# Kernel optimization log

Measured on AMD Instinct MI355X. Metric: run time of the kernel, lower is better.

## Reference

```python
import jax, jax.numpy as jnp
import numpy as np

C = 256
G = 32  # groups
EPS = 1e-5

def _xavier(key, shape, gain=1.0):
    fan_in, fan_out = shape[1], shape[0]
    a = gain * np.sqrt(6.0 / (fan_in + fan_out))
    return jax.random.uniform(key, shape, jnp.float32, -a, a)

def setup_inputs() -> dict:
    key = jax.random.key(0)
    ks = jax.random.split(key, 5)
    x = jax.random.normal(ks[0], (2, C, 16, 16, 16), jnp.float32)
    return {
        "x": x,
        "gn_gamma": jnp.ones((C,), jnp.float32),
        "gn_beta": jnp.zeros((C,), jnp.float32),
        "Wq": _xavier(ks[1], (C, C)), "bq": jnp.zeros((C,), jnp.float32),
        "Wk": _xavier(ks[2], (C, C)), "bk": jnp.zeros((C,), jnp.float32),
        "Wv": _xavier(ks[3], (C, C)), "bv": jnp.zeros((C,), jnp.float32),
        "Wp": _xavier(ks[4], (C, C), gain=1e-05), "bp": jnp.zeros((C,), jnp.float32),
    }

def reference(x, gn_gamma, gn_beta, Wq, bq, Wk, bk, Wv, bv, Wp, bp):
    B, Cc, D, H, W = x.shape
    N = D * H * W
    xf = x.reshape(B, Cc, N)  # [B, C, N]
    # GroupNorm over (C//G, N) per group
    xg = xf.reshape(B, G, Cc // G, N)
    mu = jnp.mean(xg, axis=(2, 3), keepdims=True)
    var = jnp.var(xg, axis=(2, 3), keepdims=True)
    h = ((xg - mu) * jax.lax.rsqrt(var + EPS)).reshape(B, Cc, N)
    h = h * gn_gamma[None, :, None] + gn_beta[None, :, None]
    # 1x1x1 convs == channel matmuls
    q = jnp.einsum('oc,bcn->bno', Wq, h) + bq  # [B, N, C]
    k = jnp.einsum('oc,bcn->bon', Wk, h) + bk[None, :, None]  # [B, C, N]
    v = jnp.einsum('oc,bcn->bno', Wv, h) + bv  # [B, N, C]
    scale = float(Cc) ** (-0.5)
    w = jnp.einsum('bnc,bcm->bnm', q, k) * scale  # [B, N, N]
    w = jax.nn.softmax(w, axis=-1)
    a = jnp.einsum('bnm,bmc->bnc', w, v)  # [B, N, C]
    out = jnp.einsum('oc,bnc->bon', Wp, a) + bp[None, :, None]  # [B, C, N]
    return x + out.reshape(B, Cc, D, H, W)
```

## Files before the change

### kernel.cpp

```cpp
#include <hip/hip_runtime.h>
#include <stdint.h>

#define B_ 2
#define C_ 256
#define N_ 4096
#define EPS_ 1e-5f

typedef short short8 __attribute__((ext_vector_type(8)));
typedef float f32x4 __attribute__((ext_vector_type(4)));
typedef float f32x16 __attribute__((ext_vector_type(16)));
typedef long long i64;

static __device__ __forceinline__ unsigned short f2bf(float f) {
    union { float f; unsigned int u; } v; v.f = f;
    unsigned int r = v.u + 0x7FFF + ((v.u >> 16) & 1);
    return (unsigned short)(r >> 16);
}
static __device__ __forceinline__ float bf2f(unsigned short u) {
    union { unsigned int u; float f; } v; v.u = ((unsigned int)u) << 16;
    return v.f;
}
static __device__ __forceinline__ unsigned char f2fp8(float f) {
    return (unsigned char)(__builtin_amdgcn_cvt_pk_fp8_f32(f, f, 0, false) & 0xff);
}
static __device__ __forceinline__ unsigned int pack4_bf8(float a, float b, float c, float d) {
    int v = __builtin_amdgcn_cvt_pk_bf8_f32(a, b, 0, false);
    v = __builtin_amdgcn_cvt_pk_bf8_f32(c, d, v, true);
    return (unsigned int)v;
}
static __device__ __forceinline__ i64 mk64(unsigned int lo, unsigned int hi) {
    return (i64)(((unsigned long long)hi << 32) | (unsigned long long)lo);
}

__global__ __launch_bounds__(256) void prep(
    const float* __restrict__ x, float2* __restrict__ stats,
    const float* __restrict__ Wq, const float* __restrict__ Wk,
    const float* __restrict__ Wv, const float* __restrict__ Wp,
    ushort* __restrict__ o)
{
    __shared__ float as_[4], as2_[4];
    if (blockIdx.x < 64) {
        const float4* p = reinterpret_cast<const float4*>(x + (size_t)blockIdx.x * 32768);
        float s = 0.f, ss = 0.f;
        for (int i = threadIdx.x; i < 8192; i += 256) {
            float4 v = p[i];
            s  += v.x + v.y + v.z + v.w;
            ss += v.x*v.x + v.y*v.y + v.z*v.z + v.w*v.w;
        }
        for (int m = 32; m; m >>= 1) { s += __shfl_down(s, m, 64); ss += __shfl_down(ss, m, 64); }
        int w = threadIdx.x >> 6;
        if ((threadIdx.x & 63) == 0) { as_[w] = s; as2_[w] = ss; }
        __syncthreads();
        if (threadIdx.x == 0) {
            float S = as_[0]+as_[1]+as_[2]+as_[3], SS = as2_[0]+as2_[1]+as2_[2]+as2_[3];
            float mu = S / 32768.f;
            float var = SS / 32768.f - mu*mu;
            stats[blockIdx.x] = make_float2(mu, rsqrtf(var + EPS_));
        }
    } else {
        int t = (blockIdx.x - 64) * 256 + threadIdx.x;
        int idx = t * 4;
        int sel = idx >> 16;
        const float* src = sel == 0 ? Wq : sel == 1 ? Wk : sel == 2 ? Wv : Wp;
        float4 v = *reinterpret_cast<const float4*>(src + (idx & 65535));
        ushort4 r; r.x = f2bf(v.x); r.y = f2bf(v.y); r.z = f2bf(v.z); r.w = f2bf(v.w);
        *reinterpret_cast<ushort4*>(o + idx) = r;
    }
}

__global__ void gnorm_t(const float* __restrict__ x, const float2* __restrict__ stats,
                        const float* __restrict__ gamma, const float* __restrict__ beta,
                        ushort* __restrict__ ht) {
    __shared__ float tile[32][33];
    int b = blockIdx.z, n0 = blockIdx.x * 32, c0 = blockIdx.y * 32;
    int tx = threadIdx.x, ty = threadIdx.y;
    #pragma unroll
    for (int i = 0; i < 4; i++) {
        int c = c0 + ty + i*8;
        float2 st = stats[b*32 + (c >> 3)];
        float v = x[((size_t)(b*C_ + c))*N_ + n0 + tx];
        tile[ty + i*8][tx] = (v - st.x) * st.y * gamma[c] + beta[c];
    }
    __syncthreads();
    #pragma unroll
    for (int i = 0; i < 4; i++) {
        int n = n0 + ty + i*8;
        ht[((size_t)(b*N_ + n))*C_ + c0 + tx] = f2bf(tile[tx][ty + i*8]);
    }
}

__global__ __launch_bounds__(256) void qkvproj(
    const ushort* __restrict__ ht, const ushort* __restrict__ wq,
    const ushort* __restrict__ wk, const ushort* __restrict__ wv,
    const float* __restrict__ bq, const float* __restrict__ bk, const float* __restrict__ bv,
    unsigned char* __restrict__ qo, unsigned char* __restrict__ ko, unsigned char* __restrict__ vo)
{
    __shared__ ushort sA[64][72], sBq[64][72], sBk[64][72], sBv[64][72];
    int bz = blockIdx.z;
    const ushort* Ab = ht + (size_t)bz * N_ * C_;
    int i0 = blockIdx.x * 64, j0 = blockIdx.y * 64;
    int tid = threadIdx.x, w = tid >> 6, lane = tid & 63, lr = lane & 15, lg = lane >> 4;
    f32x4 aq[4] = {}, ak[4] = {}, av[4] = {};
    for (int ks = 0; ks < 256; ks += 64) {
        #pragma unroll
        for (int it = 0; it < 2; it++) {
            int ch = tid + it*256;
            int row = ch >> 3, cc = ch & 7;
            *reinterpret_cast<uint4*>(&sA[row][cc*8]) =
                *reinterpret_cast<const uint4*>(Ab + ((size_t)(i0 + row))*256 + ks + cc*8);
            *reinterpret_cast<uint4*>(&sBq[row][cc*8]) =
                *reinterpret_cast<const uint4*>(wq + ((size_t)(j0 + row))*256 + ks + cc*8);
            *reinterpret_cast<uint4*>(&sBk[row][cc*8]) =
                *reinterpret_cast<const uint4*>(wk + ((size_t)(j0 + row))*256 + ks + cc*8);
            *reinterpret_cast<uint4*>(&sBv[row][cc*8]) =
                *reinterpret_cast<const uint4*>(wv + ((size_t)(j0 + row))*256 + ks + cc*8);
        }
        __syncthreads();
        #pragma unroll
        for (int kc = 0; kc < 2; kc++) {
            short8 af = *reinterpret_cast<const short8*>(&sA[w*16 + lr][kc*32 + lg*8]);
            #pragma unroll
            for (int cb = 0; cb < 4; cb++) {
                short8 b1 = *reinterpret_cast<const short8*>(&sBq[cb*16 + lr][kc*32 + lg*8]);
                short8 b2 = *reinterpret_cast<const short8*>(&sBk[cb*16 + lr][kc*32 + lg*8]);
                short8 b3 = *reinterpret_cast<const short8*>(&sBv[cb*16 + lr][kc*32 + lg*8]);
                aq[cb] = __builtin_amdgcn_mfma_f32_16x16x32_bf16(af, b1, aq[cb], 0, 0, 0);
                ak[cb] = __builtin_amdgcn_mfma_f32_16x16x32_bf16(af, b2, ak[cb], 0, 0, 0);
                av[cb] = __builtin_amdgcn_mfma_f32_16x16x32_bf16(af, b3, av[cb], 0, 0, 0);
            }
        }
        __syncthreads();
    }
    #pragma unroll
    for (int cb = 0; cb < 4; cb++) {
        #pragma unroll
        for (int r = 0; r < 4; r++) {
            int i = i0 + w*16 + lg*4 + r;
            int j = j0 + cb*16 + lr;
            size_t oidx = ((size_t)(bz*N_ + i))*256 + j;
            qo[oidx] = f2fp8(aq[cb][r] + bq[j]);
            ko[oidx] = f2fp8(ak[cb][r] + bk[j]);
            vo[((size_t)bz*C_ + j)*N_ + i] = f2fp8(av[cb][r] + bv[j]);
        }
    }
}

#define FLASH_LDS 70656
__global__ __launch_bounds__(256, 2) void flash10(
    const unsigned char* __restrict__ q, const unsigned char* __restrict__ k,
    const unsigned char* __restrict__ vT,
    ushort* __restrict__ Opart, float* __restrict__ lsum, ushort* __restrict__ aout, int nsplit)
{
    extern __shared__ char smem[];
    int b = blockIdx.z, s = blockIdx.y, qt = blockIdx.x;
    int tid = threadIdx.x, w = tid >> 6, lane = tid & 63;
    int l31 = lane & 31, hi = lane >> 5;
    int nrow0 = qt*128 + w*32;
    const unsigned char* kB = k  + (size_t)b * N_ * 256;
    const unsigned char* vB = vT + (size_t)b * 256 * N_;

    i64 qf[16];
    #pragma unroll
    for (int kc = 0; kc < 16; kc++)
        qf[kc] = *reinterpret_cast<const i64*>(
            q + ((size_t)(b*N_) + nrow0 + l31)*256 + kc*16 + hi*8);

    f32x16 oacc[8] = {};
    float lp = 0.f;

    int tiles = 64 / nsplit;
    int t0 = s * tiles;

    char* kbuf0 = smem;
    char* vbuf0 = smem + 33792;

    int koff[4], kd[4], voff[4], vd[4];
    #pragma unroll
    for (int i = 0; i < 4; i++) {
        int row = w*16 + i*4 + (lane >> 4);
        koff[i] = (t0*64 + row)*256 + (lane & 15)*16;
        kd[i]   = row*264 + (lane & 15)*16;
        int c = w*64 + i*16 + (lane >> 2);
        voff[i] = c*4096 + t0*64 + (lane & 3)*16;
        vd[i]   = c*72 + (lane & 3)*16;
    }

    uint4 kreg[4], vreg[4];
    auto loadKV = [&]() {
        #pragma unroll
        for (int i = 0; i < 4; i++) { kreg[i] = *reinterpret_cast<const uint4*>(kB + koff[i]); koff[i] += 16384; }
        #pragma unroll
        for (int i = 0; i < 4; i++) { vreg[i] = *reinterpret_cast<const uint4*>(vB + voff[i]); voff[i] += 64; }
    };
    auto writeKV = [&](int sel) {
        #pragma unroll
        for (int i = 0; i < 4; i++) {
            char* p = kbuf0 + sel*16896 + kd[i];
            *reinterpret_cast<uint2*>(p)     = make_uint2(kreg[i].x, kreg[i].y);
            *reinterpret_cast<uint2*>(p + 8) = make_uint2(kreg[i].z, kreg[i].w);
        }
        #pragma unroll
        for (int i = 0; i < 4; i++) {
            char* p = vbuf0 + sel*18432 + vd[i];
            *reinterpret_cast<uint2*>(p)     = make_uint2(vreg[i].x, vreg[i].y);
            *reinterpret_cast<uint2*>(p + 8) = make_uint2(vreg[i].z, vreg[i].w);
        }
    };

    loadKV();
    writeKV(0);
    __syncthreads();
    int sel = 0;

    for (int ti = 0; ti < tiles; ti++) {
        bool more = (ti + 1 < tiles);
        if (more) loadKV();

        const char* kb_ = kbuf0 + sel*16896;
        f32x16 s0 = {}, s1 = {};
        __builtin_amdgcn_s_setprio(1);
        #pragma unroll
        for (int kc = 0; kc < 16; kc++) {
            i64 ka0 = *reinterpret_cast<const i64*>(kb_ + l31*264        + kc*16 + hi*8);
            i64 ka1 = *reinterpret_cast<const i64*>(kb_ + (l31+32)*264   + kc*16 + hi*8);
            s0 = __builtin_amdgcn_mfma_f32_32x32x16_fp8_fp8(ka0, qf[kc], s0, 0, 0, 0);
            s1 = __builtin_amdgcn_mfma_f32_32x32x16_fp8_fp8(ka1, qf[kc], s1, 0, 0, 0);
        }
        __builtin_amdgcn_s_setprio(0);

        float e0[16], e1[16];
        #pragma unroll
        for (int r = 0; r < 16; r++) {
            e0[r] = __expf(fminf(s0[r]*0.0625f, 10.5f));
            e1[r] = __expf(fminf(s1[r]*0.0625f, 10.5f));
            lp += e0[r] + e1[r];
        }
        unsigned p0 = pack4_bf8(e0[0],e0[1],e0[2],e0[3]);
        unsigned p1 = pack4_bf8(e0[4],e0[5],e0[6],e0[7]);
        unsigned p2 = pack4_bf8(e0[8],e0[9],e0[10],e0[11]);
        unsigned p3 = pack4_bf8(e0[12],e0[13],e0[14],e0[15]);
        unsigned t0_ = pack4_bf8(e1[0],e1[1],e1[2],e1[3]);
        unsigned t1_ = pack4_bf8(e1[4],e1[5],e1[6],e1[7]);
        unsigned t2_ = pack4_bf8(e1[8],e1[9],e1[10],e1[11]);
        unsigned t3_ = pack4_bf8(e1[12],e1[13],e1[14],e1[15]);
        unsigned xp0 = (unsigned)__shfl_xor((int)p0, 32, 64);
        unsigned xp1 = (unsigned)__shfl_xor((int)p1, 32, 64);
        unsigned xp2 = (unsigned)__shfl_xor((int)p2, 32, 64);
        unsigned xp3 = (unsigned)__shfl_xor((int)p3, 32, 64);
        unsigned xt0 = (unsigned)__shfl_xor((int)t0_, 32, 64);
        unsigned xt1 = (unsigned)__shfl_xor((int)t1_, 32, 64);
        unsigned xt2 = (unsigned)__shfl_xor((int)t2_, 32, 64);
        unsigned xt3 = (unsigned)__shfl_xor((int)t3_, 32, 64);
        i64 A0 = mk64(hi ? xp1 : p0,  hi ? p1 : xp0);
        i64 A1 = mk64(hi ? xp3 : p2,  hi ? p3 : xp2);
        i64 A2 = mk64(hi ? xt1 : t0_, hi ? t1_ : xt0);
        i64 A3 = mk64(hi ? xt3 : t2_, hi ? t3_ : xt2);

        const char* vb_ = vbuf0 + sel*18432;
        __builtin_amdgcn_s_setprio(1);
        #pragma unroll
        for (int cb = 0; cb < 8; cb++) {
            const char* vrow = vb_ + (cb*32 + l31)*72;
            i64 bv0 = *reinterpret_cast<const i64*>(vrow + 0*16  + hi*8);
            oacc[cb] = __builtin_amdgcn_mfma_f32_32x32x16_bf8_fp8(A0, bv0, oacc[cb], 0, 0, 0);
            i64 bv1 = *reinterpret_cast<const i64*>(vrow + 1*16  + hi*8);
            oacc[cb] = __builtin_amdgcn_mfma_f32_32x32x16_bf8_fp8(A1, bv1, oacc[cb], 0, 0, 0);
            i64 bv2 = *reinterpret_cast<const i64*>(vrow + 2*16  + hi*8);
            oacc[cb] = __builtin_amdgcn_mfma_f32_32x32x16_bf8_fp8(A2, bv2, oacc[cb], 0, 0, 0);
            i64 bv3 = *reinterpret_cast<const i64*>(vrow + 3*16  + hi*8);
            oacc[cb] = __builtin_amdgcn_mfma_f32_32x32x16_bf8_fp8(A3, bv3, oacc[cb], 0, 0, 0);
        }
        __builtin_amdgcn_s_setprio(0);

        if (more) writeKV(sel ^ 1);
        __syncthreads();
        sel ^= 1;
    }

    lp += __shfl_xor(lp, 32, 64);

    if (nsplit == 1) {
        float inv = 1.f / lp;
        #pragma unroll
        for (int r = 0; r < 16; r++) {
            int R = (r & 3) + 8*(r >> 2) + 4*hi;
            #pragma unroll
            for (int cb = 0; cb < 8; cb++)
                aout[((size_t)(b*N_) + nrow0 + R)*256 + cb*32 + l31] = f2bf(oacc[cb][r] * inv);
        }
    } else {
        size_t obase = ((size_t)(b*nsplit + s)*N_ + nrow0) * 256;
        #pragma unroll
        for (int r = 0; r < 16; r++) {
            int R = (r & 3) + 8*(r >> 2) + 4*hi;
            #pragma unroll
            for (int cb = 0; cb < 8; cb++)
                Opart[obase + (size_t)R*256 + cb*32 + l31] = f2bf(oacc[cb][r]);
        }
        if (hi == 0)
            lsum[(size_t)(b*nsplit + s)*N_ + nrow0 + l31] = lp;
    }
}

__global__ void combine2(const ushort* __restrict__ Opart, const float* __restrict__ lsum,
                         ushort* __restrict__ aout, int nsplit) {
    int g = threadIdx.x >> 6, lane = threadIdx.x & 63;
    int idx = blockIdx.x*4 + g;
    int b = idx >> 12, n = idx & 4095;
    float L = 0.f;
    for (int s2 = 0; s2 < nsplit; s2++) L += lsum[(size_t)(b*nsplit + s2)*N_ + n];
    float inv = 1.f / L;
    float a0 = 0.f, a1 = 0.f, a2 = 0.f, a3 = 0.f;
    for (int s2 = 0; s2 < nsplit; s2++) {
        ushort4 o = *reinterpret_cast<const ushort4*>(
            Opart + ((size_t)(b*nsplit + s2)*N_ + n)*256 + lane*4);
        a0 += bf2f(o.x); a1 += bf2f(o.y); a2 += bf2f(o.z); a3 += bf2f(o.w);
    }
    ushort4 r; r.x = f2bf(a0*inv); r.y = f2bf(a1*inv); r.z = f2bf(a2*inv); r.w = f2bf(a3*inv);
    *reinterpret_cast<ushort4*>(aout + (size_t)idx*256 + lane*4) = r;
}

__global__ __launch_bounds__(256) void pgemm(
    const ushort* __restrict__ A, const ushort* __restrict__ Bm,
    const float* __restrict__ bias, const float* __restrict__ resid,
    float* __restrict__ outp, long bBatch, long oBatch)
{
    __shared__ ushort sA[64][72];
    __shared__ ushort sB[64][72];
    int bz = blockIdx.z;
    const ushort* Bb = Bm + (size_t)bBatch * bz;
    int i0 = blockIdx.x * 64, j0 = blockIdx.y * 64;
    int tid = threadIdx.x, w = tid >> 6, lane = tid & 63, lr = lane & 15, lg = lane >> 4;
    f32x4 acc[4] = {};
    for (int ks = 0; ks < 256; ks += 64) {
        #pragma unroll
        for (int it = 0; it < 2; it++) {
            int ch = tid + it*256;
            int row = ch >> 3, cc = ch & 7;
            *reinterpret_cast<uint4*>(&sA[row][cc*8]) =
                *reinterpret_cast<const uint4*>(A + ((size_t)(i0 + row))*256 + ks + cc*8);
            *reinterpret_cast<uint4*>(&sB[row][cc*8]) =
                *reinterpret_cast<const uint4*>(Bb + ((size_t)(j0 + row))*256 + ks + cc*8);
        }
        __syncthreads();
        #pragma unroll
        for (int kc = 0; kc < 2; kc++) {
            short8 af = *reinterpret_cast<const short8*>(&sA[w*16 + lr][kc*32 + lg*8]);
            #pragma unroll
            for (int cb = 0; cb < 4; cb++) {
                short8 bf = *reinterpret_cast<const short8*>(&sB[cb*16 + lr][kc*32 + lg*8]);
                acc[cb] = __builtin_amdgcn_mfma_f32_16x16x32_bf16(af, bf, acc[cb], 0, 0, 0);
            }
        }
        __syncthreads();
    }
    #pragma unroll
    for (int cb = 0; cb < 4; cb++) {
        #pragma unroll
        for (int r = 0; r < 4; r++) {
            int i = i0 + w*16 + lg*4 + r;
            int j = j0 + cb*16 + lr;
            size_t oidx = (size_t)oBatch*bz + (size_t)i*N_ + j;
            outp[oidx] = acc[cb][r] + bias[i] + resid[oidx];
        }
    }
}

extern "C" void kernel_launch(void* const* d_in, const int* in_sizes, int n_in,
                              void* d_out, int out_size, void* d_ws, size_t ws_size,
                              hipStream_t stream) {
    const float* x     = (const float*)d_in[0];
    const float* gamma = (const float*)d_in[1];
    const float* beta  = (const float*)d_in[2];
    const float* Wq = (const float*)d_in[3]; const float* bq = (const float*)d_in[4];
    const float* Wk = (const float*)d_in[5]; const float* bk = (const float*)d_in[6];
    const float* Wv = (const float*)d_in[7]; const float* bv = (const float*)d_in[8];
    const float* Wp = (const float*)d_in[9]; const float* bp = (const float*)d_in[10];
    float* out = (float*)d_out;

    char* ws = (char*)d_ws;
    float2* stats = (float2*)ws;
    ushort* wqb = (ushort*)(ws + 1024);
    ushort* wkb = wqb + 65536;
    ushort* wvb = wkb + 65536;
    ushort* wpb = wvb + 65536;
    ushort* ht  = (ushort*)(ws + 1024 + 524288);
    const size_t NB = (size_t)B_ * N_ * C_;
    unsigned char* qb  = (unsigned char*)(ht + NB);
    unsigned char* kb8 = qb  + NB;
    unsigned char* vTb = kb8 + NB;
    ushort* ab = (ushort*)(vTb + NB);
    char* after = (char*)(ab + NB);
    float*  lsum  = (float*)after;
    ushort* Opart = (ushort*)(after + 262144);

    int nsplit = (ws_size >= (size_t)48*1024*1024) ? 8 : 4;

    hipFuncSetAttribute((const void*)flash10, hipFuncAttributeMaxDynamicSharedMemorySize,
                        FLASH_LDS);

    prep<<<320, 256, 0, stream>>>(x, stats, Wq, Wk, Wv, Wp, wqb);
    gnorm_t<<<dim3(128, 8, 2), dim3(32, 8), 0, stream>>>(x, stats, gamma, beta, ht);
    qkvproj<<<dim3(64, 4, 2), 256, 0, stream>>>(ht, wqb, wkb, wvb, bq, bk, bv, qb, kb8, vTb);
    flash10<<<dim3(32, nsplit, 2), 256, FLASH_LDS, stream>>>(qb, kb8, vTb, Opart, lsum, ab, nsplit);
    combine2<<<2048, 256, 0, stream>>>(Opart, lsum, ab, nsplit);
    pgemm<<<dim3(4, 64, 2), 256, 0, stream>>>(wpb, ab, bp, x, out, (long)N_*C_, (long)C_*N_);
}
```

Measured before the change: 87.48 us.

## Interleave QK and PV halves in flash loop, use exp2, stage V transpose in LDS

The flash kernel now computes the two 32-key score halves separately, so exp and PV MMA for the first half can overlap with work on the second. The setprio hints are removed, and the exp is rewritten as exp2f with a folded log2e scale. The nsplit==1 path is dropped. In qkvproj, the transposed V output is staged through an LDS tile so it is written as coalesced 16-byte stores instead of scattered single-byte stores.

Measured after the change: 85.05 us. 2.8% less time.

```diff
diff --git a/kernel.cpp b/kernel.cpp
--- a/kernel.cpp
+++ b/kernel.cpp
@@ -31,6 +31,8 @@
 static __device__ __forceinline__ i64 mk64(unsigned int lo, unsigned int hi) {
     return (i64)(((unsigned long long)hi << 32) | (unsigned long long)lo);
 }
+#define EXPSCALE 0.09016844f
+#define EXPCLAMP 15.148f
 
 __global__ __launch_bounds__(256) void prep(
     const float* __restrict__ x, float2* __restrict__ stats,
@@ -96,6 +98,7 @@
     unsigned char* __restrict__ qo, unsigned char* __restrict__ ko, unsigned char* __restrict__ vo)
 {
     __shared__ ushort sA[64][72], sBq[64][72], sBk[64][72], sBv[64][72];
+    __shared__ __align__(16) unsigned char vtile[64*80];
     int bz = blockIdx.z;
     const ushort* Ab = ht + (size_t)bz * N_ * C_;
     int i0 = blockIdx.x * 64, j0 = blockIdx.y * 64;
@@ -140,16 +143,22 @@
             size_t oidx = ((size_t)(bz*N_ + i))*256 + j;
             qo[oidx] = f2fp8(aq[cb][r] + bq[j]);
             ko[oidx] = f2fp8(ak[cb][r] + bk[j]);
-            vo[((size_t)bz*C_ + j)*N_ + i] = f2fp8(av[cb][r] + bv[j]);
-        }
+            vtile[(cb*16 + lr)*80 + (w*16 + lg*4 + r)] = f2fp8(av[cb][r] + bv[j]);
+        }
+    }
+    __syncthreads();
+    {
+        int cl = tid >> 2, chk = (tid & 3) * 16;
+        uint4 vv = *reinterpret_cast<const uint4*>(&vtile[cl*80 + chk]);
+        *reinterpret_cast<uint4*>(vo + ((size_t)bz*C_ + j0 + cl)*N_ + i0 + chk) = vv;
     }
 }
 
 #define FLASH_LDS 70656
-__global__ __launch_bounds__(256, 2) void flash10(
+__global__ __launch_bounds__(256, 2) void flash11(
     const unsigned char* __restrict__ q, const unsigned char* __restrict__ k,
     const unsigned char* __restrict__ vT,
-    ushort* __restrict__ Opart, float* __restrict__ lsum, ushort* __restrict__ aout, int nsplit)
+    ushort* __restrict__ Opart, float* __restrict__ lsum, int nsplit)
 {
     extern __shared__ char smem[];
     int b = blockIdx.z, s = blockIdx.y, qt = blockIdx.x;
@@ -217,60 +226,72 @@
         if (more) loadKV();
 
         const char* kb_ = kbuf0 + sel*16896;
-        f32x16 s0 = {}, s1 = {};
-        __builtin_amdgcn_s_setprio(1);
+        const char* vb_ = vbuf0 + sel*18432;
+
+        f32x16 s0 = {};
         #pragma unroll
         for (int kc = 0; kc < 16; kc++) {
-            i64 ka0 = *reinterpret_cast<const i64*>(kb_ + l31*264        + kc*16 + hi*8);
-            i64 ka1 = *reinterpret_cast<const i64*>(kb_ + (l31+32)*264   + kc*16 + hi*8);
+            i64 ka0 = *reinterpret_cast<const i64*>(kb_ + l31*264 + kc*16 + hi*8);
             s0 = __builtin_amdgcn_mfma_f32_32x32x16_fp8_fp8(ka0, qf[kc], s0, 0, 0, 0);
+        }
+        f32x16 s1 = {};
+        #pragma unroll
+        for (int kc = 0; kc < 16; kc++) {
+            i64 ka1 = *reinterpret_cast<const i64*>(kb_ + (l31+32)*264 + kc*16 + hi*8);
             s1 = __builtin_amdgcn_mfma_f32_32x32x16_fp8_fp8(ka1, qf[kc], s1, 0, 0, 0);
         }
-        __builtin_amdgcn_s_setprio(0);
-
-        float e0[16], e1[16];
+
+        float e0[16];
         #pragma unroll
         for (int r = 0; r < 16; r++) {
-            e0[r] = __expf(fminf(s0[r]*0.0625f, 10.5f));
-            e1[r] = __expf(fminf(s1[r]*0.0625f, 10.5f));
-            lp += e0[r] + e1[r];
+            e0[r] = exp2f(fminf(s0[r]*EXPSCALE, EXPCLAMP));
+            lp += e0[r];
         }
         unsigned p0 = pack4_bf8(e0[0],e0[1],e0[2],e0[3]);
         unsigned p1 = pack4_bf8(e0[4],e0[5],e0[6],e0[7]);
         unsigned p2 = pack4_bf8(e0[8],e0[9],e0[10],e0[11]);
         unsigned p3 = pack4_bf8(e0[12],e0[13],e0[14],e0[15]);
+        unsigned xp0 = (unsigned)__shfl_xor((int)p0, 32, 64);
+        unsigned xp1 = (unsigned)__shfl_xor((int)p1, 32, 64);
+        unsigned xp2 = (unsigned)__shfl_xor((int)p2, 32, 64);
+        unsigned xp3 = (unsigned)__shfl_xor((int)p3, 32, 64);
+        i64 A0 = mk64(hi ? xp1 : p0,  hi ? p1 : xp0);
+        i64 A1 = mk64(hi ? xp3 : p2,  hi ? p3 : xp2);
+
+        #pragma unroll
+        for (int cb = 0; cb < 8; cb++) {
+            const char* vrow = vb_ + (cb*32 + l31)*72;
+            i64 bv0 = *reinterpret_cast<const i64*>(vrow + 0*16 + hi*8);
+            oacc[cb] = __builtin_amdgcn_mfma_f32_32x32x16_bf8_fp8(A0, bv0, oacc[cb], 0, 0, 0);
+            i64 bv1 = *reinterpret_cast<const i64*>(vrow + 1*16 + hi*8);
+            oacc[cb] = __builtin_amdgcn_mfma_f32_32x32x16_bf8_fp8(A1, bv1, oacc[cb], 0, 0, 0);
+        }
+
+        float e1[16];
+        #pragma unroll
+        for (int r = 0; r < 16; r++) {
+            e1[r] = exp2f(fminf(s1[r]*EXPSCALE, EXPCLAMP));
+            lp += e1[r];
+        }
         unsigned t0_ = pack4_bf8(e1[0],e1[1],e1[2],e1[3]);
         unsigned t1_ = pack4_bf8(e1[4],e1[5],e1[6],e1[7]);
         unsigned t2_ = pack4_bf8(e1[8],e1[9],e1[10],e1[11]);
         unsigned t3_ = pack4_bf8(e1[12],e1[13],e1[14],e1[15]);
-        unsigned xp0 = (unsigned)__shfl_xor((int)p0, 32, 64);
-        unsigned xp1 = (unsigned)__shfl_xor((int)p1, 32, 64);
-        unsigned xp2 = (unsigned)__shfl_xor((int)p2, 32, 64);
-        unsigned xp3 = (unsigned)__shfl_xor((int)p3, 32, 64);
         unsigned xt0 = (unsigned)__shfl_xor((int)t0_, 32, 64);
         unsigned xt1 = (unsigned)__shfl_xor((int)t1_, 32, 64);
         unsigned xt2 = (unsigned)__shfl_xor((int)t2_, 32, 64);
         unsigned xt3 = (unsigned)__shfl_xor((int)t3_, 32, 64);
-        i64 A0 = mk64(hi ? xp1 : p0,  hi ? p1 : xp0);
-        i64 A1 = mk64(hi ? xp3 : p2,  hi ? p3 : xp2);
         i64 A2 = mk64(hi ? xt1 : t0_, hi ? t1_ : xt0);
         i64 A3 = mk64(hi ? xt3 : t2_, hi ? t3_ : xt2);
 
-        const char* vb_ = vbuf0 + sel*18432;
-        __builtin_amdgcn_s_setprio(1);
         #pragma unroll
         for (int cb = 0; cb < 8; cb++) {
             const char* vrow = vb_ + (cb*32 + l31)*72;
-            i64 bv0 = *reinterpret_cast<const i64*>(vrow + 0*16  + hi*8);
-            oacc[cb] = __builtin_amdgcn_mfma_f32_32x32x16_bf8_fp8(A0, bv0, oacc[cb], 0, 0, 0);
-            i64 bv1 = *reinterpret_cast<const i64*>(vrow + 1*16  + hi*8);
-            oacc[cb] = __builtin_amdgcn_mfma_f32_32x32x16_bf8_fp8(A1, bv1, oacc[cb], 0, 0, 0);
-            i64 bv2 = *reinterpret_cast<const i64*>(vrow + 2*16  + hi*8);
+            i64 bv2 = *reinterpret_cast<const i64*>(vrow + 2*16 + hi*8);
             oacc[cb] = __builtin_amdgcn_mfma_f32_32x32x16_bf8_fp8(A2, bv2, oacc[cb], 0, 0, 0);
-            i64 bv3 = *reinterpret_cast<const i64*>(vrow + 3*16  + hi*8);
+            i64 bv3 = *reinterpret_cast<const i64*>(vrow + 3*16 + hi*8);
             oacc[cb] = __builtin_amdgcn_mfma_f32_32x32x16_bf8_fp8(A3, bv3, oacc[cb], 0, 0, 0);
         }
-        __builtin_amdgcn_s_setprio(0);
 
         if (more) writeKV(sel ^ 1);
         __syncthreads();
@@ -279,27 +300,16 @@
 
     lp += __shfl_xor(lp, 32, 64);
 
-    if (nsplit == 1) {
-        float inv = 1.f / lp;
-        #pragma unroll
-        for (int r = 0; r < 16; r++) {
-            int R = (r & 3) + 8*(r >> 2) + 4*hi;
-            #pragma unroll
-            for (int cb = 0; cb < 8; cb++)
-                aout[((size_t)(b*N_) + nrow0 + R)*256 + cb*32 + l31] = f2bf(oacc[cb][r] * inv);
-        }
-    } else {
-        size_t obase = ((size_t)(b*nsplit + s)*N_ + nrow0) * 256;
-        #pragma unroll
-        for (int r = 0; r < 16; r++) {
-            int R = (r & 3) + 8*(r >> 2) + 4*hi;
-            #pragma unroll
-            for (int cb = 0; cb < 8; cb++)
-                Opart[obase + (size_t)R*256 + cb*32 + l31] = f2bf(oacc[cb][r]);
-        }
-        if (hi == 0)
-            lsum[(size_t)(b*nsplit + s)*N_ + nrow0 + l31] = lp;
-    }
+    size_t obase = ((size_t)(b*nsplit + s)*N_ + nrow0) * 256;
+    #pragma unroll
+    for (int r = 0; r < 16; r++) {
+        int R = (r & 3) + 8*(r >> 2) + 4*hi;
+        #pragma unroll
+        for (int cb = 0; cb < 8; cb++)
+            Opart[obase + (size_t)R*256 + cb*32 + l31] = f2bf(oacc[cb][r]);
+    }
+    if (hi == 0)
+        lsum[(size_t)(b*nsplit + s)*N_ + nrow0 + l31] = lp;
 }
 
 __global__ void combine2(const ushort* __restrict__ Opart, const float* __restrict__ lsum,
@@ -396,13 +406,13 @@
 
     int nsplit = (ws_size >= (size_t)48*1024*1024) ? 8 : 4;
 
-    hipFuncSetAttribute((const void*)flash10, hipFuncAttributeMaxDynamicSharedMemorySize,
+    hipFuncSetAttribute((const void*)flash11, hipFuncAttributeMaxDynamicSharedMemorySize,
                         FLASH_LDS);
 
     prep<<<320, 256, 0, stream>>>(x, stats, Wq, Wk, Wv, Wp, wqb);
     gnorm_t<<<dim3(128, 8, 2), dim3(32, 8), 0, stream>>>(x, stats, gamma, beta, ht);
     qkvproj<<<dim3(64, 4, 2), 256, 0, stream>>>(ht, wqb, wkb, wvb, bq, bk, bv, qb, kb8, vTb);
-    flash10<<<dim3(32, nsplit, 2), 256, FLASH_LDS, stream>>>(qb, kb8, vTb, Opart, lsum, ab, nsplit);
+    flash11<<<dim3(32, nsplit, 2), 256, FLASH_LDS, stream>>>(qb, kb8, vTb, Opart, lsum, nsplit);
     combine2<<<2048, 256, 0, stream>>>(Opart, lsum, ab, nsplit);
     pgemm<<<dim3(4, 64, 2), 256, 0, stream>>>(wpb, ab, bp, x, out, (long)N_*C_, (long)C_*N_);
 }
```

## Fuse split-KV combine into output projection and coalesce V-transpose stores

Applied to the files above, without the earlier changes.

Removes the separate combine kernel: the projection GEMM now sums the per-split partial outputs and divides by the summed softmax denominators while loading its B tile, and no intermediate attention-output buffer is kept. Separately, qkvproj stages the transposed V tile in shared memory and writes it out as 16-byte coalesced stores instead of scattered byte stores. The fused GEMM rereads all split partials once per output-channel block (4x across blockIdx.x), so the partial-sum traffic is duplicated in exchange for one fewer launch and one fewer round trip through memory. The workspace threshold for choosing 8 splits is also lowered.

New measurement: 96.21 us. +10.0%, slower.

```diff
diff --git a/kernel.cpp b/kernel.cpp
--- a/kernel.cpp
+++ b/kernel.cpp
@@ -96,6 +96,7 @@
     unsigned char* __restrict__ qo, unsigned char* __restrict__ ko, unsigned char* __restrict__ vo)
 {
     __shared__ ushort sA[64][72], sBq[64][72], sBk[64][72], sBv[64][72];
+    __shared__ __align__(16) unsigned char vtile[64*80];
     int bz = blockIdx.z;
     const ushort* Ab = ht + (size_t)bz * N_ * C_;
     int i0 = blockIdx.x * 64, j0 = blockIdx.y * 64;
@@ -140,8 +141,14 @@
             size_t oidx = ((size_t)(bz*N_ + i))*256 + j;
             qo[oidx] = f2fp8(aq[cb][r] + bq[j]);
             ko[oidx] = f2fp8(ak[cb][r] + bk[j]);
-            vo[((size_t)bz*C_ + j)*N_ + i] = f2fp8(av[cb][r] + bv[j]);
-        }
+            vtile[(cb*16 + lr)*80 + (w*16 + lg*4 + r)] = f2fp8(av[cb][r] + bv[j]);
+        }
+    }
+    __syncthreads();
+    {
+        int cl = tid >> 2, chk = (tid & 3) * 16;
+        uint4 vv = *reinterpret_cast<const uint4*>(&vtile[cl*80 + chk]);
+        *reinterpret_cast<uint4*>(vo + ((size_t)bz*C_ + j0 + cl)*N_ + i0 + chk) = vv;
     }
 }
 
@@ -149,7 +156,7 @@
 __global__ __launch_bounds__(256, 2) void flash10(
     const unsigned char* __restrict__ q, const unsigned char* __restrict__ k,
     const unsigned char* __restrict__ vT,
-    ushort* __restrict__ Opart, float* __restrict__ lsum, ushort* __restrict__ aout, int nsplit)
+    ushort* __restrict__ Opart, float* __restrict__ lsum, int nsplit)
 {
     extern __shared__ char smem[];
     int b = blockIdx.z, s = blockIdx.y, qt = blockIdx.x;
@@ -279,58 +286,37 @@
 
     lp += __shfl_xor(lp, 32, 64);
 
-    if (nsplit == 1) {
-        float inv = 1.f / lp;
-        #pragma unroll
-        for (int r = 0; r < 16; r++) {
-            int R = (r & 3) + 8*(r >> 2) + 4*hi;
-            #pragma unroll
-            for (int cb = 0; cb < 8; cb++)
-                aout[((size_t)(b*N_) + nrow0 + R)*256 + cb*32 + l31] = f2bf(oacc[cb][r] * inv);
-        }
-    } else {
-        size_t obase = ((size_t)(b*nsplit + s)*N_ + nrow0) * 256;
-        #pragma unroll
-        for (int r = 0; r < 16; r++) {
-            int R = (r & 3) + 8*(r >> 2) + 4*hi;
-            #pragma unroll
-            for (int cb = 0; cb < 8; cb++)
-                Opart[obase + (size_t)R*256 + cb*32 + l31] = f2bf(oacc[cb][r]);
-        }
-        if (hi == 0)
-            lsum[(size_t)(b*nsplit + s)*N_ + nrow0 + l31] = lp;
-    }
-}
-
-__global__ void combine2(const ushort* __restrict__ Opart, const float* __restrict__ lsum,
-                         ushort* __restrict__ aout, int nsplit) {
-    int g = threadIdx.x >> 6, lane = threadIdx.x & 63;
-    int idx = blockIdx.x*4 + g;
-    int b = idx >> 12, n = idx & 4095;
-    float L = 0.f;
-    for (int s2 = 0; s2 < nsplit; s2++) L += lsum[(size_t)(b*nsplit + s2)*N_ + n];
-    float inv = 1.f / L;
-    float a0 = 0.f, a1 = 0.f, a2 = 0.f, a3 = 0.f;
-    for (int s2 = 0; s2 < nsplit; s2++) {
-        ushort4 o = *reinterpret_cast<const ushort4*>(
-            Opart + ((size_t)(b*nsplit + s2)*N_ + n)*256 + lane*4);
-        a0 += bf2f(o.x); a1 += bf2f(o.y); a2 += bf2f(o.z); a3 += bf2f(o.w);
-    }
-    ushort4 r; r.x = f2bf(a0*inv); r.y = f2bf(a1*inv); r.z = f2bf(a2*inv); r.w = f2bf(a3*inv);
-    *reinterpret_cast<ushort4*>(aout + (size_t)idx*256 + lane*4) = r;
-}
-
-__global__ __launch_bounds__(256) void pgemm(
-    const ushort* __restrict__ A, const ushort* __restrict__ Bm,
-    const float* __restrict__ bias, const float* __restrict__ resid,
-    float* __restrict__ outp, long bBatch, long oBatch)
+    size_t obase = ((size_t)(b*nsplit + s)*N_ + nrow0) * 256;
+    #pragma unroll
+    for (int r = 0; r < 16; r++) {
+        int R = (r & 3) + 8*(r >> 2) + 4*hi;
+        #pragma unroll
+        for (int cb = 0; cb < 8; cb++)
+            Opart[obase + (size_t)R*256 + cb*32 + l31] = f2bf(oacc[cb][r]);
+    }
+    if (hi == 0)
+        lsum[(size_t)(b*nsplit + s)*N_ + nrow0 + l31] = lp;
+}
+
+__global__ __launch_bounds__(256) void pgemm2(
+    const ushort* __restrict__ Wp_, const ushort* __restrict__ Opart,
+    const float* __restrict__ lsum, const float* __restrict__ bias,
+    const float* __restrict__ resid, float* __restrict__ outp, int nsplit)
 {
     __shared__ ushort sA[64][72];
     __shared__ ushort sB[64][72];
     int bz = blockIdx.z;
-    const ushort* Bb = Bm + (size_t)bBatch * bz;
     int i0 = blockIdx.x * 64, j0 = blockIdx.y * 64;
     int tid = threadIdx.x, w = tid >> 6, lane = tid & 63, lr = lane & 15, lg = lane >> 4;
+
+    int r0 = tid >> 3;
+    float L0 = 0.f, L1 = 0.f;
+    for (int s2 = 0; s2 < nsplit; s2++) {
+        L0 += lsum[(size_t)(bz*nsplit + s2)*N_ + j0 + r0];
+        L1 += lsum[(size_t)(bz*nsplit + s2)*N_ + j0 + r0 + 32];
+    }
+    float invL0 = 1.f / L0, invL1 = 1.f / L1;
+
     f32x4 acc[4] = {};
     for (int ks = 0; ks < 256; ks += 64) {
         #pragma unroll
@@ -338,9 +324,19 @@
             int ch = tid + it*256;
             int row = ch >> 3, cc = ch & 7;
             *reinterpret_cast<uint4*>(&sA[row][cc*8]) =
-                *reinterpret_cast<const uint4*>(A + ((size_t)(i0 + row))*256 + ks + cc*8);
-            *reinterpret_cast<uint4*>(&sB[row][cc*8]) =
-                *reinterpret_cast<const uint4*>(Bb + ((size_t)(j0 + row))*256 + ks + cc*8);
+                *reinterpret_cast<const uint4*>(Wp_ + ((size_t)(i0 + row))*256 + ks + cc*8);
+            float a8[8] = {};
+            for (int s2 = 0; s2 < nsplit; s2++) {
+                short8 v = *reinterpret_cast<const short8*>(
+                    Opart + ((size_t)(bz*nsplit + s2)*N_ + j0 + row)*256 + ks + cc*8);
+                #pragma unroll
+                for (int e = 0; e < 8; e++) a8[e] += bf2f((unsigned short)v[e]);
+            }
+            float invL = it ? invL1 : invL0;
+            short8 outv;
+            #pragma unroll
+            for (int e = 0; e < 8; e++) outv[e] = (short)f2bf(a8[e] * invL);
+            *reinterpret_cast<short8*>(&sB[row][cc*8]) = outv;
         }
         __syncthreads();
         #pragma unroll
@@ -360,7 +356,7 @@
         for (int r = 0; r < 4; r++) {
             int i = i0 + w*16 + lg*4 + r;
             int j = j0 + cb*16 + lr;
-            size_t oidx = (size_t)oBatch*bz + (size_t)i*N_ + j;
+            size_t oidx = (size_t)bz*C_*N_ + (size_t)i*N_ + j;
             outp[oidx] = acc[cb][r] + bias[i] + resid[oidx];
         }
     }
@@ -389,12 +385,11 @@
     unsigned char* qb  = (unsigned char*)(ht + NB);
     unsigned char* kb8 = qb  + NB;
     unsigned char* vTb = kb8 + NB;
-    ushort* ab = (ushort*)(vTb + NB);
-    char* after = (char*)(ab + NB);
+    char* after = (char*)(vTb + NB);
     float*  lsum  = (float*)after;
     ushort* Opart = (ushort*)(after + 262144);
 
-    int nsplit = (ws_size >= (size_t)48*1024*1024) ? 8 : 4;
+    int nsplit = (ws_size >= (size_t)44*1024*1024) ? 8 : 4;
 
     hipFuncSetAttribute((const void*)flash10, hipFuncAttributeMaxDynamicSharedMemorySize,
                         FLASH_LDS);
@@ -402,7 +397,6 @@
     prep<<<320, 256, 0, stream>>>(x, stats, Wq, Wk, Wv, Wp, wqb);
     gnorm_t<<<dim3(128, 8, 2), dim3(32, 8), 0, stream>>>(x, stats, gamma, beta, ht);
     qkvproj<<<dim3(64, 4, 2), 256, 0, stream>>>(ht, wqb, wkb, wvb, bq, bk, bv, qb, kb8, vTb);
-    flash10<<<dim3(32, nsplit, 2), 256, FLASH_LDS, stream>>>(qb, kb8, vTb, Opart, lsum, ab, nsplit);
-    combine2<<<2048, 256, 0, stream>>>(Opart, lsum, ab, nsplit);
-    pgemm<<<dim3(4, 64, 2), 256, 0, stream>>>(wpb, ab, bp, x, out, (long)N_*C_, (long)C_*N_);
-}
+    flash10<<<dim3(32, nsplit, 2), 256, FLASH_LDS, stream>>>(qb, kb8, vTb, Opart, lsum, nsplit);
+    pgemm2<<<dim3(4, 64, 2), 256, 0, stream>>>(wpb, Opart, lsum, bp, x, out, nsplit);
+}
```
